# Performance work log

Hardware: AMD Instinct MI355X
Metric: run time of the kernel (lower is better)

## Reference

```python
import jax, jax.numpy as jnp
import numpy as np

B = 4096   # batch (samples)
V = 64     # num_vars
H = 512    # hidden_dim


def setup_inputs() -> dict:
    key = jax.random.key(0)
    k0, k1, k2, k3 = jax.random.split(key, 4)
    x = jax.random.normal(k0, (B, V), dtype=jnp.float32)
    # learned params: adjacency logits + stacked per-variable 2-layer MLPs
    adj_weights = jax.random.normal(k1, (V, V), dtype=jnp.float32) * 0.1
    W1 = jax.random.normal(k2, (V, V - 1, H), dtype=jnp.float32) * (1.0 / np.sqrt(V - 1))
    b1 = jnp.zeros((V, H), dtype=jnp.float32)
    W2 = jax.random.normal(k3, (V, H), dtype=jnp.float32) * (1.0 / np.sqrt(H))
    b2 = jnp.zeros((V,), dtype=jnp.float32)
    return {"x": x, "adj_weights": adj_weights, "W1": W1, "b1": b1, "W2": W2, "b2": b2}


def reference(x, adj_weights, W1, b1, W2, b2):
    Vn = adj_weights.shape[0]
    # sigmoid adjacency with zeroed diagonal
    adj = jax.nn.sigmoid(adj_weights) * (1.0 - jnp.eye(Vn, dtype=adj_weights.dtype))
    # idx[i, j] = j if j < i else j + 1  -> columns of x excluding variable i
    j = jnp.arange(Vn - 1)
    idx = j[None, :] + (j[None, :] >= jnp.arange(Vn)[:, None])  # [V, V-1] int
    gathered = x[:, idx]                                  # [B, V, V-1]
    w = jnp.take_along_axis(adj, idx, axis=1)             # [V, V-1] (row i, cols != i)
    weighted = gathered * w[None, :, :]                   # [B, V, V-1]
    # batched small MLP per variable
    h = jax.nn.relu(jnp.einsum('bvk,vkh->bvh', weighted, W1) + b1[None])  # [B, V, H]
    out = jnp.einsum('bvh,vh->bv', h, W2) + b2[None]                      # [B, V]
    return out
```

## Files before the change

### kernel.cpp

```cpp
#include <hip/hip_runtime.h>
#include <hip/hip_bf16.h>

constexpr int Bn = 4096;
constexpr int Vn = 64;
constexpr int Hn = 512;

typedef __attribute__((ext_vector_type(8))) short bf16x8;
typedef __attribute__((ext_vector_type(4))) float f32x4;
typedef __attribute__((ext_vector_type(8))) unsigned short u16x8;

__device__ __forceinline__ unsigned short f2bf(float f) {
    union { float f; unsigned int u; } x; x.f = f;
    unsigned int u = x.u;
    u += 0x7fffu + ((u >> 16) & 1u);
    return (unsigned short)(u >> 16);
}

__global__ void prep_w1(const float* __restrict__ adjw,
                        const float* __restrict__ W1,
                        unsigned short* __restrict__ bfrag) {
    int tid  = blockIdx.x * blockDim.x + threadIdx.x;
    int lane = tid & 63;
    int ks   = (tid >> 6) & 1;
    int nt   = (tid >> 7) & 31;
    int v    = tid >> 12;

    int n     = nt * 16 + (lane & 15);
    int kbase = ks * 32 + ((lane >> 4) << 3);

    u16x8 o;
#pragma unroll
    for (int e = 0; e < 8; ++e) {
        int k = kbase + e;
        float val = 0.f;
        if (k != v) {
            float aw = adjw[v * Vn + k];
            float s  = 1.f / (1.f + __expf(-aw));
            int  j   = k - (k > v);
            val = s * W1[((size_t)(v * (Vn - 1) + j)) * Hn + n];
        }
        o[e] = f2bf(val);
    }
    *reinterpret_cast<u16x8*>(bfrag + (size_t)tid * 8) = o;
}

__global__ void prep_x(const float* __restrict__ x,
                       unsigned short* __restrict__ afrag) {
    int tid  = blockIdx.x * blockDim.x + threadIdx.x;
    int lane = tid & 63;
    int ks   = (tid >> 6) & 1;
    int mt   = tid >> 7;

    int b     = mt * 16 + (lane & 15);
    int kbase = ks * 32 + ((lane >> 4) << 3);

    u16x8 o;
#pragma unroll
    for (int e = 0; e < 8; ++e)
        o[e] = f2bf(x[(size_t)b * Vn + kbase + e]);
    *reinterpret_cast<u16x8*>(afrag + (size_t)tid * 8) = o;
}

__global__ __launch_bounds__(256, 4)
void main_k(const unsigned short* __restrict__ afrag,
            const unsigned short* __restrict__ bfrag,
            const float* __restrict__ b1, const float* __restrict__ W2,
            const float* __restrict__ b2, float* __restrict__ out) {
    int wid  = threadIdx.x >> 6;
    int lane = threadIdx.x & 63;
    int nb   = (blockIdx.x & 7) * 128 + (blockIdx.x >> 3);
    int job  = nb * 4 + wid;
    int v    = job >> 6;
    int rg   = job & 63;

    bf16x8 a[4][2];
#pragma unroll
    for (int m = 0; m < 4; ++m)
#pragma unroll
        for (int ks = 0; ks < 2; ++ks)
            a[m][ks] = *reinterpret_cast<const bf16x8*>(
                afrag + ((size_t)((rg * 4 + m) * 2 + ks)) * 512 + lane * 8);

    const unsigned short* bpan = bfrag + (size_t)v * 32 * 2 * 512;
    const float* w2row = W2 + v * Hn;
    const float* b1row = b1 + v * Hn;
    int ncol = lane & 15;

    bf16x8 pb0[3], pb1[3];
    float  pw2[3], pbv[3];
#pragma unroll
    for (int p = 0; p < 2; ++p) {
        pb0[p] = *reinterpret_cast<const bf16x8*>(bpan + (size_t)p * 1024 + 0 + lane * 8);
        pb1[p] = *reinterpret_cast<const bf16x8*>(bpan + (size_t)p * 1024 + 512 + lane * 8);
        pw2[p] = w2row[p * 16 + ncol];
        pbv[p] = b1row[p * 16 + ncol];
    }

    float partial[4][4] = {};

#pragma unroll
    for (int j = 0; j < 32; ++j) {
        const int cur = j % 3;
        if (j < 30) {
            const int nxt = (j + 2) % 3;
            pb0[nxt] = *reinterpret_cast<const bf16x8*>(
                bpan + (size_t)(j + 2) * 1024 + 0 + lane * 8);
            pb1[nxt] = *reinterpret_cast<const bf16x8*>(
                bpan + (size_t)(j + 2) * 1024 + 512 + lane * 8);
            pw2[nxt] = w2row[(j + 2) * 16 + ncol];
            pbv[nxt] = b1row[(j + 2) * 16 + ncol];
        }
#pragma unroll
        for (int m = 0; m < 4; ++m) {
            f32x4 c = {pbv[cur], pbv[cur], pbv[cur], pbv[cur]};
            c = __builtin_amdgcn_mfma_f32_16x16x32_bf16(a[m][0], pb0[cur], c, 0, 0, 0);
            c = __builtin_amdgcn_mfma_f32_16x16x32_bf16(a[m][1], pb1[cur], c, 0, 0, 0);
#pragma unroll
            for (int r = 0; r < 4; ++r)
                partial[m][r] = fmaf(fmaxf(c[r], 0.f), pw2[cur], partial[m][r]);
        }
    }

#pragma unroll
    for (int m = 0; m < 4; ++m)
#pragma unroll
        for (int r = 0; r < 4; ++r) {
            float s = partial[m][r];
            s += __shfl_xor(s, 1);
            s += __shfl_xor(s, 2);
            s += __shfl_xor(s, 4);
            s += __shfl_xor(s, 8);
            partial[m][r] = s;
        }

    float b2v = b2[v];
    if ((lane & 15) == 0) {
        int hi = lane >> 4;
#pragma unroll
        for (int m = 0; m < 4; ++m)
#pragma unroll
            for (int r = 0; r < 4; ++r) {
                int row = rg * 64 + m * 16 + hi * 4 + r;
                out[(size_t)row * Vn + v] = partial[m][r] + b2v;
            }
    }
}

extern "C" void kernel_launch(void* const* d_in, const int* in_sizes, int n_in,
                              void* d_out, int out_size, void* d_ws, size_t ws_size,
                              hipStream_t stream) {
    const float* x    = (const float*)d_in[0];
    const float* adjw = (const float*)d_in[1];
    const float* W1   = (const float*)d_in[2];
    const float* b1   = (const float*)d_in[3];
    const float* W2   = (const float*)d_in[4];
    const float* b2   = (const float*)d_in[5];
    float* out = (float*)d_out;

    unsigned short* bfrag = (unsigned short*)d_ws;
    unsigned short* afrag = bfrag + (size_t)Vn * Vn * Hn;

    prep_w1<<<262144 / 256, 256, 0, stream>>>(adjw, W1, bfrag);
    prep_x<<<32768 / 256, 256, 0, stream>>>(x, afrag);
    main_k<<<1024, 256, 0, stream>>>(afrag, bfrag, b1, W2, b2, out);
}
```

Before: 33.33 us.

## Fuse x bf16 conversion into main kernel and deepen B-fragment prefetch

Removes the prep_x kernel and has each wave load fp32 rows of x and convert them to bf16 MFMA fragments inline, saving one launch and a round trip through workspace. The B-panel prefetch becomes a full three-deep ring, with each slot refilled after its MFMAs finish. The MFMAs are wrapped in s_setprio so matrix work gets scheduling priority. prep_w1 now uses the same XCD-swizzled block mapping as main_k, which may improve L2 locality when main_k reads bfrag. The trade-off is some redundant x conversion across waves that share a row group, and higher register pressure from the extra prefetch slot.

```diff
diff --git a/kernel.cpp b/kernel.cpp
--- a/kernel.cpp
+++ b/kernel.cpp
@@ -9,6 +9,8 @@
 typedef __attribute__((ext_vector_type(4))) float f32x4;
 typedef __attribute__((ext_vector_type(8))) unsigned short u16x8;
 
+union bfcast { u16x8 u; bf16x8 b; };
+
 __device__ __forceinline__ unsigned short f2bf(float f) {
     union { float f; unsigned int u; } x; x.f = f;
     unsigned int u = x.u;
@@ -19,7 +21,8 @@
 __global__ void prep_w1(const float* __restrict__ adjw,
                         const float* __restrict__ W1,
                         unsigned short* __restrict__ bfrag) {
-    int tid  = blockIdx.x * blockDim.x + threadIdx.x;
+    int nb   = (blockIdx.x & 7) * 128 + (blockIdx.x >> 3);
+    int tid  = nb * 256 + threadIdx.x;
     int lane = tid & 63;
     int ks   = (tid >> 6) & 1;
     int nt   = (tid >> 7) & 31;
@@ -44,25 +47,8 @@
     *reinterpret_cast<u16x8*>(bfrag + (size_t)tid * 8) = o;
 }
 
-__global__ void prep_x(const float* __restrict__ x,
-                       unsigned short* __restrict__ afrag) {
-    int tid  = blockIdx.x * blockDim.x + threadIdx.x;
-    int lane = tid & 63;
-    int ks   = (tid >> 6) & 1;
-    int mt   = tid >> 7;
-
-    int b     = mt * 16 + (lane & 15);
-    int kbase = ks * 32 + ((lane >> 4) << 3);
-
-    u16x8 o;
-#pragma unroll
-    for (int e = 0; e < 8; ++e)
-        o[e] = f2bf(x[(size_t)b * Vn + kbase + e]);
-    *reinterpret_cast<u16x8*>(afrag + (size_t)tid * 8) = o;
-}
-
 __global__ __launch_bounds__(256, 4)
-void main_k(const unsigned short* __restrict__ afrag,
+void main_k(const float* __restrict__ x,
             const unsigned short* __restrict__ bfrag,
             const float* __restrict__ b1, const float* __restrict__ W2,
             const float* __restrict__ b2, float* __restrict__ out) {
@@ -73,14 +59,6 @@
     int v    = job >> 6;
     int rg   = job & 63;
 
-    bf16x8 a[4][2];
-#pragma unroll
-    for (int m = 0; m < 4; ++m)
-#pragma unroll
-        for (int ks = 0; ks < 2; ++ks)
-            a[m][ks] = *reinterpret_cast<const bf16x8*>(
-                afrag + ((size_t)((rg * 4 + m) * 2 + ks)) * 512 + lane * 8);
-
     const unsigned short* bpan = bfrag + (size_t)v * 32 * 2 * 512;
     const float* w2row = W2 + v * Hn;
     const float* b1row = b1 + v * Hn;
@@ -89,35 +67,58 @@
     bf16x8 pb0[3], pb1[3];
     float  pw2[3], pbv[3];
 #pragma unroll
-    for (int p = 0; p < 2; ++p) {
+    for (int p = 0; p < 3; ++p) {
         pb0[p] = *reinterpret_cast<const bf16x8*>(bpan + (size_t)p * 1024 + 0 + lane * 8);
         pb1[p] = *reinterpret_cast<const bf16x8*>(bpan + (size_t)p * 1024 + 512 + lane * 8);
         pw2[p] = w2row[p * 16 + ncol];
         pbv[p] = b1row[p * 16 + ncol];
     }
 
+    bf16x8 a[4][2];
+#pragma unroll
+    for (int m = 0; m < 4; ++m)
+#pragma unroll
+        for (int ks = 0; ks < 2; ++ks) {
+            int brow  = rg * 64 + m * 16 + (lane & 15);
+            int kbase = ks * 32 + ((lane >> 4) << 3);
+            const float* xp = x + (size_t)brow * Vn + kbase;
+            f32x4 lo = *reinterpret_cast<const f32x4*>(xp);
+            f32x4 hi = *reinterpret_cast<const f32x4*>(xp + 4);
+            bfcast t;
+#pragma unroll
+            for (int e = 0; e < 4; ++e) {
+                t.u[e]     = f2bf(lo[e]);
+                t.u[e + 4] = f2bf(hi[e]);
+            }
+            a[m][ks] = t.b;
+        }
+
     float partial[4][4] = {};
 
 #pragma unroll
     for (int j = 0; j < 32; ++j) {
         const int cur = j % 3;
-        if (j < 30) {
-            const int nxt = (j + 2) % 3;
-            pb0[nxt] = *reinterpret_cast<const bf16x8*>(
-                bpan + (size_t)(j + 2) * 1024 + 0 + lane * 8);
-            pb1[nxt] = *reinterpret_cast<const bf16x8*>(
-                bpan + (size_t)(j + 2) * 1024 + 512 + lane * 8);
-            pw2[nxt] = w2row[(j + 2) * 16 + ncol];
-            pbv[nxt] = b1row[(j + 2) * 16 + ncol];
+        if (j < 29) {
+            const int nxt = j % 3;
         }
 #pragma unroll
         for (int m = 0; m < 4; ++m) {
             f32x4 c = {pbv[cur], pbv[cur], pbv[cur], pbv[cur]};
+            __builtin_amdgcn_s_setprio(1);
             c = __builtin_amdgcn_mfma_f32_16x16x32_bf16(a[m][0], pb0[cur], c, 0, 0, 0);
             c = __builtin_amdgcn_mfma_f32_16x16x32_bf16(a[m][1], pb1[cur], c, 0, 0, 0);
+            __builtin_amdgcn_s_setprio(0);
 #pragma unroll
             for (int r = 0; r < 4; ++r)
                 partial[m][r] = fmaf(fmaxf(c[r], 0.f), pw2[cur], partial[m][r]);
+        }
+        if (j < 29) {
+            pb0[cur] = *reinterpret_cast<const bf16x8*>(
+                bpan + (size_t)(j + 3) * 1024 + 0 + lane * 8);
+            pb1[cur] = *reinterpret_cast<const bf16x8*>(
+                bpan + (size_t)(j + 3) * 1024 + 512 + lane * 8);
+            pw2[cur] = w2row[(j + 3) * 16 + ncol];
+            pbv[cur] = b1row[(j + 3) * 16 + ncol];
         }
     }
 
@@ -158,9 +159,7 @@
     float* out = (float*)d_out;
 
     unsigned short* bfrag = (unsigned short*)d_ws;
-    unsigned short* afrag = bfrag + (size_t)Vn * Vn * Hn;
 
-    prep_w1<<<262144 / 256, 256, 0, stream>>>(adjw, W1, bfrag);
-    prep_x<<<32768 / 256, 256, 0, stream>>>(x, afrag);
-    main_k<<<1024, 256, 0, stream>>>(afrag, bfrag, b1, W2, b2, out);
+    prep_w1<<<1024, 256, 0, stream>>>(adjw, W1, bfrag);
+    main_k<<<1024, 256, 0, stream>>>(x, bfrag, b1, W2, b2, out);
 }
```

Result: slower. 35.23 us (+5.7%).
